# Kernel tuning notes

Hardware: AMD Instinct MI355X
Metric: run time of the kernel (lower is better)

The kernel has to match this reference:

```python
import jax, jax.numpy as jnp
import numpy as np

N = 100000
E = 1600000
NEG_SLOPE = 0.2
EPS = 1e-16


def gat_layer(x, src, dst, w, W, a_src, a_dst, b):
    # x: [N, Cin] -> h: [N, Cout]
    h = x @ W
    alpha_src = h @ a_src  # [N]
    alpha_dst = h @ a_dst  # [N]
    # per-edge score: alpha_j + alpha_i, leaky relu, edge-weight adjustment
    alpha = alpha_src[src] + alpha_dst[dst]
    alpha = jax.nn.leaky_relu(alpha, NEG_SLOPE)
    alpha = alpha + (1.0 - 1.0 / w)
    # segment softmax over destination nodes
    m = jax.ops.segment_max(alpha, dst, num_segments=N)
    ea = jnp.exp(alpha - m[dst])
    denom = jax.ops.segment_sum(ea, dst, num_segments=N)
    alpha = ea / (denom[dst] + EPS)
    # scatter-add aggregation of weighted source features
    out = jax.ops.segment_sum(h[src] * alpha[:, None], dst, num_segments=N)
    return out + b


def setup_inputs() -> dict:
    key = jax.random.key(0)
    ks = jax.random.split(key, 12)
    return {
        "x": jax.random.normal(ks[0], (N, 128), dtype=jnp.float32),
        "edge_index": jax.random.randint(ks[1], (2, E), 0, N, dtype=jnp.int64)
        if jax.config.jax_enable_x64 else jax.random.randint(ks[1], (2, E), 0, N, dtype=jnp.int32),
        "edge_weight": jax.random.uniform(ks[2], (E,), dtype=jnp.float32, minval=0.5, maxval=1.5),
        "W1": jax.random.normal(ks[3], (128, 64), dtype=jnp.float32) * 0.08,
        "a_src1": jax.random.normal(ks[4], (64,), dtype=jnp.float32) * 0.1,
        "a_dst1": jax.random.normal(ks[5], (64,), dtype=jnp.float32) * 0.1,
        "b1": jax.random.normal(ks[6], (64,), dtype=jnp.float32) * 0.01,
        "W2": jax.random.normal(ks[7], (64, 7), dtype=jnp.float32) * 0.12,
        "a_src2": jax.random.normal(ks[8], (7,), dtype=jnp.float32) * 0.1,
        "a_dst2": jax.random.normal(ks[9], (7,), dtype=jnp.float32) * 0.1,
        "b2": jax.random.normal(ks[10], (7,), dtype=jnp.float32) * 0.01,
    }


def reference(x, edge_index, edge_weight, W1, a_src1, a_dst1, b1, W2, a_src2, a_dst2, b2):
    # add self loops with edge weight fill_value=1.0 (GATConv default behavior)
    loop = jnp.arange(N, dtype=edge_index.dtype)
    src = jnp.concatenate([edge_index[0], loop])
    dst = jnp.concatenate([edge_index[1], loop])
    w = jnp.concatenate([edge_weight, jnp.ones((N,), dtype=edge_weight.dtype)])
    h = gat_layer(x, src, dst, w, W1, a_src1, a_dst1, b1)
    h = jax.nn.relu(h)  # dropout is identity in eval mode
    out = gat_layer(h, src, dst, w, W2, a_src2, a_dst2, b2)
    return out
```

## Files before the change

kernel.cpp:

```cpp
#include <hip/hip_runtime.h>
#include <hip/hip_bf16.h>

typedef __hip_bfloat16 bf16;

#define DEPS 1e-16f
#define CAP 32
#define OVF_MAX 131072

__device__ __forceinline__ float bfu_lo(unsigned u) { return __uint_as_float(u << 16); }
__device__ __forceinline__ float bfu_hi(unsigned u) { return __uint_as_float(u & 0xffff0000u); }

__device__ __forceinline__ float dec_wt(unsigned u) {
    return (float)(u & 32767u) * (1.f / 8192.f) - 1.1f;
}

__global__ __launch_bounds__(256) void f_hist(
    const int* __restrict__ dstv, int* __restrict__ cnt,
    unsigned char* __restrict__ rank8, int E)
{
    int e = blockIdx.x * 256 + threadIdx.x;
    if (e >= E) return;
    int d = dstv[e];
    int pos = atomicAdd(&cnt[d], 1);
    rank8[e] = (unsigned char)min(pos, 255);
}

__global__ __launch_bounds__(256) void f_gemm_scat(
    const float* __restrict__ x, const float* __restrict__ W1,
    const float* __restrict__ a_src, const float* __restrict__ a_dst,
    bf16* __restrict__ h1, float* __restrict__ asrc, float* __restrict__ adst,
    const int* __restrict__ srcv, const int* __restrict__ dstv,
    const float* __restrict__ ew, const unsigned char* __restrict__ rank8,
    const int* __restrict__ cnt,
    unsigned* __restrict__ bkt, uint2* __restrict__ ovf, int* __restrict__ ovfn,
    int N, int E, int T, int gG, int gS)
{
    __shared__ __align__(16) float xl[32 * 128];
    int bid = blockIdx.x;
    int r = bid % 13, chunk = bid / 13;
    int tid = threadIdx.x;

    if (r >= 4) {
        int sb = chunk * 9 + (r - 4);
        if (sb >= gS) return;
        int e = sb * 256 + tid;
        if (e >= T) return;
        int s, d, pos; float wt;
        if (e < E) {
            s = srcv[e]; d = dstv[e]; wt = 1.f - 1.f / ew[e];
            pos = rank8[e];
        } else {
            s = d = e - E; wt = 0.f;
            pos = cnt[d];
        }
        unsigned q = (unsigned)((wt + 1.1f) * 8192.f + 0.5f);
        unsigned entry = ((unsigned)s << 15) | q;
        if (pos < CAP) {
            bkt[(size_t)d * CAP + pos] = entry;
        } else {
            int o = atomicAdd(ovfn, 1);
            if (o < OVF_MAX) { uint2 v; v.x = (unsigned)d; v.y = entry; ovf[o] = v; }
        }
        return;
    }
    int gb = chunk * 4 + r;
    if (gb >= gG) return;
    int n0 = gb * 32;
    for (int i = tid; i < 1024; i += 256) {
        int n = n0 + (i >> 5);
        float4 v = {0.f, 0.f, 0.f, 0.f};
        if (n < N) v = ((const float4*)x)[(size_t)n * 32 + (i & 31)];
        ((float4*)xl)[i] = v;
    }
    __syncthreads();
    int w = tid >> 6, c = tid & 63;
    float sa = a_src[c], da = a_dst[c];
    float acc[8] = {0.f, 0.f, 0.f, 0.f, 0.f, 0.f, 0.f, 0.f};
    const float* Wc = W1 + c;
    for (int k4 = 0; k4 < 32; ++k4) {
        float w0 = Wc[(4 * k4 + 0) * 64];
        float w1 = Wc[(4 * k4 + 1) * 64];
        float w2 = Wc[(4 * k4 + 2) * 64];
        float w3 = Wc[(4 * k4 + 3) * 64];
        #pragma unroll
        for (int i = 0; i < 8; ++i) {
            float4 xv = ((const float4*)(xl + (w * 8 + i) * 128))[k4];
            acc[i] = fmaf(xv.x, w0, fmaf(xv.y, w1,
                     fmaf(xv.z, w2, fmaf(xv.w, w3, acc[i]))));
        }
    }
    #pragma unroll
    for (int i = 0; i < 8; ++i) {
        int n = n0 + w * 8 + i;
        float a = acc[i];
        float ps = a * sa, pd = a * da;
        #pragma unroll
        for (int o = 32; o; o >>= 1) {
            ps += __shfl_xor(ps, o);
            pd += __shfl_xor(pd, o);
        }
        if (n < N) {
            h1[(size_t)n * 64 + c] = __float2bfloat16(a);
            if (c == 0) { asrc[n] = ps; adst[n] = pd; }
        }
    }
}

__global__ __launch_bounds__(256) void f_agg1(
    const int* __restrict__ cnt, const unsigned* __restrict__ bkt,
    const uint2* __restrict__ ovf, const int* __restrict__ ovfn,
    const float* __restrict__ asrc, const float* __restrict__ adst,
    const bf16* __restrict__ h1,
    const float* __restrict__ b1, const float* __restrict__ W2,
    const float* __restrict__ a2s, const float* __restrict__ a2d,
    float* __restrict__ h2p, float* __restrict__ ad2, int N)
{
    __shared__ __align__(16) float WxT[16][68];
    __shared__ __align__(16) float b1l[64];
    __shared__ float2 eb[4][64];
    int tid = threadIdx.x;
    if (tid < 64) {
        float us = 0.f, ud = 0.f;
        #pragma unroll
        for (int c = 0; c < 7; ++c) {
            float wv = W2[tid * 7 + c];
            WxT[c][tid] = wv;
            us = fmaf(wv, a2s[c], us);
            ud = fmaf(wv, a2d[c], ud);
        }
        WxT[7][tid] = us;
        WxT[8][tid] = ud;
        #pragma unroll
        for (int r = 9; r < 16; ++r) WxT[r][tid] = 0.f;
        b1l[tid] = b1[tid];
    }
    __syncthreads();
    int d = blockIdx.x * 4 + (tid >> 6);
    int lane = tid & 63;
    if (d >= N) return;
    int lenf = cnt[d] + 1;
    int nc = min(lenf, CAP);
    size_t r0 = (size_t)d * CAP;
    float adv = adst[d];
    int g8 = lane >> 3, l8 = lane & 7;
    float2* ebw = eb[tid >> 6];
    float acc[8] = {0.f, 0.f, 0.f, 0.f, 0.f, 0.f, 0.f, 0.f};
    float sm = 0.f;
    {
        float ea = 0.f; unsigned s = 0;
        if (lane < nc) {
            unsigned u = bkt[r0 + lane];
            s = u >> 15;
            float a = asrc[s] + adv;
            a = (a > 0.f) ? a : 0.2f * a;
            ea = __expf(a + dec_wt(u));
            sm += ea;
        }
        ebw[lane] = make_float2(ea, __uint_as_float(s));
        for (int j = 0; j < nc; j += 8) {
            float2 eq = ebw[j + g8];
            float e = eq.x;
            unsigned sj = __float_as_uint(eq.y);
            uint4 hv = *(const uint4*)&h1[(size_t)sj * 64 + (l8 << 3)];
            acc[0] = fmaf(e, bfu_lo(hv.x), acc[0]);
            acc[1] = fmaf(e, bfu_hi(hv.x), acc[1]);
            acc[2] = fmaf(e, bfu_lo(hv.y), acc[2]);
            acc[3] = fmaf(e, bfu_hi(hv.y), acc[3]);
            acc[4] = fmaf(e, bfu_lo(hv.z), acc[4]);
            acc[5] = fmaf(e, bfu_hi(hv.z), acc[5]);
            acc[6] = fmaf(e, bfu_lo(hv.w), acc[6]);
            acc[7] = fmaf(e, bfu_hi(hv.w), acc[7]);
        }
    }
    if (lenf > CAP) {
        int no = min(*ovfn, OVF_MAX);
        for (int i = g8; i < no; i += 8) {
            uint2 ov = ovf[i];
            if ((int)ov.x == d) {
                unsigned u = ov.y;
                unsigned s = u >> 15;
                float a = asrc[s] + adv;
                a = (a > 0.f) ? a : 0.2f * a;
                float ea = __expf(a + dec_wt(u));
                if (l8 == 0) sm += ea;
                uint4 hv = *(const uint4*)&h1[(size_t)s * 64 + (l8 << 3)];
                acc[0] = fmaf(ea, bfu_lo(hv.x), acc[0]);
                acc[1] = fmaf(ea, bfu_hi(hv.x), acc[1]);
                acc[2] = fmaf(ea, bfu_lo(hv.y), acc[2]);
                acc[3] = fmaf(ea, bfu_hi(hv.y), acc[3]);
                acc[4] = fmaf(ea, bfu_lo(hv.z), acc[4]);
                acc[5] = fmaf(ea, bfu_hi(hv.z), acc[5]);
                acc[6] = fmaf(ea, bfu_lo(hv.w), acc[6]);
                acc[7] = fmaf(ea, bfu_hi(hv.w), acc[7]);
            }
        }
    }
    #pragma unroll
    for (int o = 32; o; o >>= 1) sm += __shfl_xor(sm, o);
    #pragma unroll
    for (int k = 0; k < 8; ++k) {
        acc[k] += __shfl_xor(acc[k], 8);
        acc[k] += __shfl_xor(acc[k], 16);
        acc[k] += __shfl_xor(acc[k], 32);
    }
    float inv = 1.f / (sm + DEPS);
    int c0 = l8 << 3;
    float4 bA = *(const float4*)&b1l[c0];
    float4 bB = *(const float4*)&b1l[c0 + 4];
    float v0 = fmaxf(fmaf(acc[0], inv, bA.x), 0.f);
    float v1 = fmaxf(fmaf(acc[1], inv, bA.y), 0.f);
    float v2 = fmaxf(fmaf(acc[2], inv, bA.z), 0.f);
    float v3 = fmaxf(fmaf(acc[3], inv, bA.w), 0.f);
    float v4 = fmaxf(fmaf(acc[4], inv, bB.x), 0.f);
    float v5 = fmaxf(fmaf(acc[5], inv, bB.y), 0.f);
    float v6 = fmaxf(fmaf(acc[6], inv, bB.z), 0.f);
    float v7 = fmaxf(fmaf(acc[7], inv, bB.w), 0.f);
    float4 wA0 = *(const float4*)&WxT[g8][c0];
    float4 wA1 = *(const float4*)&WxT[g8][c0 + 4];
    float4 wB0 = *(const float4*)&WxT[g8 + 8][c0];
    float4 wB1 = *(const float4*)&WxT[g8 + 8][c0 + 4];
    float rA = fmaf(v0, wA0.x, fmaf(v1, wA0.y, fmaf(v2, wA0.z, fmaf(v3, wA0.w,
               fmaf(v4, wA1.x, fmaf(v5, wA1.y, fmaf(v6, wA1.z, v7 * wA1.w)))))));
    float rB = fmaf(v0, wB0.x, fmaf(v1, wB0.y, fmaf(v2, wB0.z, fmaf(v3, wB0.w,
               fmaf(v4, wB1.x, fmaf(v5, wB1.y, fmaf(v6, wB1.z, v7 * wB1.w)))))));
    rA += __shfl_xor(rA, 1); rA += __shfl_xor(rA, 2); rA += __shfl_xor(rA, 4);
    rB += __shfl_xor(rB, 1); rB += __shfl_xor(rB, 2); rB += __shfl_xor(rB, 4);
    if (l8 == 0) {
        h2p[(size_t)d * 8 + g8] = rA;
        if (g8 == 0) ad2[d] = rB;
    }
}

__global__ __launch_bounds__(256) void f_agg2(
    const int* __restrict__ cnt, const unsigned* __restrict__ bkt,
    const uint2* __restrict__ ovf, const int* __restrict__ ovfn,
    const float* __restrict__ h2p, const float* __restrict__ ad2,
    const float* __restrict__ b2, float* __restrict__ out, int N)
{
    __shared__ float b2l[7];
    if (threadIdx.x < 7) b2l[threadIdx.x] = b2[threadIdx.x];
    __syncthreads();
    int lane = threadIdx.x & 63;
    int wv = threadIdx.x >> 6;
    int grp = lane >> 3, l8 = lane & 7;
    int d = blockIdx.x * 32 + wv * 8 + grp;
    bool valid = d < N;
    int lenf = 0; float adv = 0.f;
    if (valid) { lenf = cnt[d] + 1; adv = ad2[d]; }
    int nc = min(lenf, CAP);
    size_t r0 = (size_t)d * CAP;
    float sm = 0.f;
    float a0 = 0.f, a1 = 0.f, a2 = 0.f, a3 = 0.f, a4 = 0.f, a5 = 0.f, a6 = 0.f;
    for (int p = l8; p < nc; p += 8) {
        unsigned u = bkt[r0 + p];
        int s = (int)(u >> 15);
        const float* hr = &h2p[(size_t)s * 8];
        float4 A = *(const float4*)hr;
        float4 B = *(const float4*)(hr + 4);
        float a = B.w + adv;
        a = (a > 0.f) ? a : 0.2f * a;
        float ea = __expf(a + dec_wt(u));
        sm += ea;
        a0 = fmaf(ea, A.x, a0); a1 = fmaf(ea, A.y, a1);
        a2 = fmaf(ea, A.z, a2); a3 = fmaf(ea, A.w, a3);
        a4 = fmaf(ea, B.x, a4); a5 = fmaf(ea, B.y, a5);
        a6 = fmaf(ea, B.z, a6);
    }
    if (lenf > CAP) {
        int no = min(*ovfn, OVF_MAX);
        for (int i = l8; i < no; i += 8) {
            uint2 ov = ovf[i];
            if ((int)ov.x == d) {
                unsigned u = ov.y;
                int s = (int)(u >> 15);
                const float* hr = &h2p[(size_t)s * 8];
                float4 A = *(const float4*)hr;
                float4 B = *(const float4*)(hr + 4);
                float a = B.w + adv;
                a = (a > 0.f) ? a : 0.2f * a;
                float ea = __expf(a + dec_wt(u));
                sm += ea;
                a0 = fmaf(ea, A.x, a0); a1 = fmaf(ea, A.y, a1);
                a2 = fmaf(ea, A.z, a2); a3 = fmaf(ea, A.w, a3);
                a4 = fmaf(ea, B.x, a4); a5 = fmaf(ea, B.y, a5);
                a6 = fmaf(ea, B.z, a6);
            }
        }
    }
    #pragma unroll
    for (int o = 4; o; o >>= 1) {
        sm += __shfl_xor(sm, o);
        a0 += __shfl_xor(a0, o); a1 += __shfl_xor(a1, o);
        a2 += __shfl_xor(a2, o); a3 += __shfl_xor(a3, o);
        a4 += __shfl_xor(a4, o); a5 += __shfl_xor(a5, o);
        a6 += __shfl_xor(a6, o);
    }
    if (valid && l8 < 7) {
        float inv = 1.f / (sm + DEPS);
        float val = (l8 < 4) ? ((l8 < 2) ? (l8 ? a1 : a0) : ((l8 == 2) ? a2 : a3))
                             : ((l8 < 6) ? ((l8 == 4) ? a4 : a5) : a6);
        out[(size_t)d * 7 + l8] = fmaf(val, inv, b2l[l8]);
    }
}


extern "C" void kernel_launch(void* const* d_in, const int* in_sizes, int n_in,
                              void* d_out, int out_size, void* d_ws, size_t ws_size,
                              hipStream_t stream) {
    const float* x   = (const float*)d_in[0];
    const int*   ei  = (const int*)d_in[1];
    const float* ew  = (const float*)d_in[2];
    const float* W1  = (const float*)d_in[3];
    const float* as1 = (const float*)d_in[4];
    const float* ad1 = (const float*)d_in[5];
    const float* b1  = (const float*)d_in[6];
    const float* W2  = (const float*)d_in[7];
    const float* a2s = (const float*)d_in[8];
    const float* a2d = (const float*)d_in[9];
    const float* b2  = (const float*)d_in[10];

    int N = in_sizes[0] / 128;
    int E = in_sizes[1] / 2;
    int T = E + N;
    const int* srcv = ei;
    const int* dstv = ei + E;
    float* out = (float*)d_out;

    size_t A = 0;
    auto take = [&](size_t b) { size_t o = A; A = (A + b + 255) & ~(size_t)255; return o; };
    size_t o_h1   = take((size_t)N * 64 * 2);
    size_t o_bkt  = take((size_t)N * CAP * 4);
    size_t o_h2p  = take((size_t)N * 8 * 4);
    size_t o_ovf  = take((size_t)OVF_MAX * 8);
    size_t o_cnt  = take((size_t)N * 4);
    size_t o_ovfn = take(256);
    size_t o_asrc = take((size_t)N * 4);
    size_t o_adst = take((size_t)N * 4);
    size_t o_ad2  = take((size_t)N * 4);

    char* base = (char*)d_ws;
    bf16*     h1    = (bf16*)(base + o_h1);
    unsigned* bkt   = (unsigned*)(base + o_bkt);
    float*    h2p   = (float*)(base + o_h2p);
    unsigned char* rank8 = (unsigned char*)(base + o_h2p);
    uint2*    ovf   = (uint2*)(base + o_ovf);
    int*      cnt   = (int*)(base + o_cnt);
    int*      ovfn  = (int*)(base + o_ovfn);
    float*    asrc  = (float*)(base + o_asrc);
    float*    adst  = (float*)(base + o_adst);
    float*    ad2   = (float*)(base + o_ad2);

    int gE = (E + 255) / 256;
    int gG = (N + 31) / 32;
    int gS = (T + 255) / 256;
    int chunks = max((gG + 3) / 4, (gS + 8) / 9);
    int gridGS = chunks * 13;

    hipMemsetAsync(cnt, 0, (size_t)N * 4 + 256, stream);
    f_hist<<<gE, 256, 0, stream>>>(dstv, cnt, rank8, E);
    f_gemm_scat<<<gridGS, 256, 0, stream>>>(x, W1, as1, ad1, h1, asrc, adst,
                                            srcv, dstv, ew, rank8, cnt,
                                            bkt, ovf, ovfn, N, E, T, gG, gS);
    f_agg1 <<<(N + 3) / 4, 256, 0, stream>>>(cnt, bkt, ovf, ovfn, asrc, adst, h1,
                                             b1, W2, a2s, a2d, h2p, ad2, N);
    f_agg2 <<<(N + 31) / 32, 256, 0, stream>>>(cnt, bkt, ovf, ovfn, h2p, ad2, b2, out, N);
}
```

Baseline: 315.0 us.

## Fuse all stages into one cooperative persistent kernel with grid syncs

```diff
diff --git a/kernel.cpp b/kernel.cpp
--- a/kernel.cpp
+++ b/kernel.cpp
@@ -1,6 +1,8 @@
 #include <hip/hip_runtime.h>
 #include <hip/hip_bf16.h>
-
+#include <hip/hip_cooperative_groups.h>
+
+namespace cg = cooperative_groups;
 typedef __hip_bfloat16 bf16;
 
 #define DEPS 1e-16f
@@ -14,264 +16,250 @@
     return (float)(u & 32767u) * (1.f / 8192.f) - 1.1f;
 }
 
-__global__ __launch_bounds__(256) void f_hist(
-    const int* __restrict__ dstv, int* __restrict__ cnt,
-    unsigned char* __restrict__ rank8, int E)
+__global__ __launch_bounds__(256) void f_mega(
+    const float* __restrict__ x, const int* __restrict__ srcv,
+    const int* __restrict__ dstv, const float* __restrict__ ew,
+    const float* __restrict__ W1, const float* __restrict__ as1,
+    const float* __restrict__ ad1, const float* __restrict__ b1,
+    const float* __restrict__ W2, const float* __restrict__ a2s,
+    const float* __restrict__ a2d, const float* __restrict__ b2,
+    bf16* __restrict__ h1, unsigned* __restrict__ bkt,
+    float* __restrict__ h2p, unsigned char* __restrict__ rank8,
+    uint2* __restrict__ ovf, int* __restrict__ cnt, int* __restrict__ ovfn,
+    float* __restrict__ asrc, float* __restrict__ adst, float* __restrict__ ad2,
+    float* __restrict__ out, int N, int E, int T)
 {
-    int e = blockIdx.x * 256 + threadIdx.x;
-    if (e >= E) return;
-    int d = dstv[e];
-    int pos = atomicAdd(&cnt[d], 1);
-    rank8[e] = (unsigned char)min(pos, 255);
-}
-
-__global__ __launch_bounds__(256) void f_gemm_scat(
-    const float* __restrict__ x, const float* __restrict__ W1,
-    const float* __restrict__ a_src, const float* __restrict__ a_dst,
-    bf16* __restrict__ h1, float* __restrict__ asrc, float* __restrict__ adst,
-    const int* __restrict__ srcv, const int* __restrict__ dstv,
-    const float* __restrict__ ew, const unsigned char* __restrict__ rank8,
-    const int* __restrict__ cnt,
-    unsigned* __restrict__ bkt, uint2* __restrict__ ovf, int* __restrict__ ovfn,
-    int N, int E, int T, int gG, int gS)
-{
-    __shared__ __align__(16) float xl[32 * 128];
-    int bid = blockIdx.x;
-    int r = bid % 13, chunk = bid / 13;
+    cg::grid_group grid = cg::this_grid();
+    __shared__ __align__(16) char smem[16896];
     int tid = threadIdx.x;
-
-    if (r >= 4) {
-        int sb = chunk * 9 + (r - 4);
-        if (sb >= gS) return;
-        int e = sb * 256 + tid;
-        if (e >= T) return;
-        int s, d, pos; float wt;
-        if (e < E) {
-            s = srcv[e]; d = dstv[e]; wt = 1.f - 1.f / ew[e];
-            pos = rank8[e];
-        } else {
-            s = d = e - E; wt = 0.f;
-            pos = cnt[d];
-        }
+    int gid = blockIdx.x * 256 + tid;
+    int nth = gridDim.x * 256;
+
+    for (int i = gid; i < N; i += nth) cnt[i] = 0;
+    if (gid == 0) *ovfn = 0;
+    grid.sync();
+
+    {
+        float* xl = (float*)smem;
+        int gG = (N + 31) >> 5;
+        int gH = (T + 255) >> 8;
+        int chunks = max((gG + 3) / 4, (gH + 8) / 9);
+        int V = chunks * 13;
+        for (int vb = blockIdx.x; vb < V; vb += gridDim.x) {
+            int r = vb % 13, chunk = vb / 13;
+            if (r >= 4) {
+                int hb = chunk * 9 + (r - 4);
+                if (hb >= gH) continue;
+                int e = hb * 256 + tid;
+                if (e >= T) continue;
+                if (e < E) {
+                    int d = dstv[e];
+                    int pos = atomicAdd(&cnt[d], 1);
+                    rank8[e] = (unsigned char)min(pos, 255);
+                } else {
+                    int d = e - E;
+                    unsigned q = (unsigned)((0.f + 1.1f) * 8192.f + 0.5f);
+                    bkt[(size_t)d * CAP] = ((unsigned)d << 15) | q;
+                }
+            } else {
+                int gb = chunk * 4 + r;
+                if (gb >= gG) continue;
+                int n0 = gb * 32;
+                for (int i = tid; i < 1024; i += 256) {
+                    int n = n0 + (i >> 5);
+                    float4 v = {0.f, 0.f, 0.f, 0.f};
+                    if (n < N) v = ((const float4*)x)[(size_t)n * 32 + (i & 31)];
+                    ((float4*)xl)[i] = v;
+                }
+                __syncthreads();
+                int wv = tid >> 6, c = tid & 63;
+                float sa = as1[c], da = ad1[c];
+                float acc[8] = {0.f, 0.f, 0.f, 0.f, 0.f, 0.f, 0.f, 0.f};
+                const float* Wc = W1 + c;
+                for (int k4 = 0; k4 < 32; ++k4) {
+                    float w0 = Wc[(4 * k4 + 0) * 64];
+                    float w1 = Wc[(4 * k4 + 1) * 64];
+                    float w2 = Wc[(4 * k4 + 2) * 64];
+                    float w3 = Wc[(4 * k4 + 3) * 64];
+                    #pragma unroll
+                    for (int i = 0; i < 8; ++i) {
+                        float4 xv = ((const float4*)(xl + (wv * 8 + i) * 128))[k4];
+                        acc[i] = fmaf(xv.x, w0, fmaf(xv.y, w1,
+                                 fmaf(xv.z, w2, fmaf(xv.w, w3, acc[i]))));
+                    }
+                }
+                #pragma unroll
+                for (int i = 0; i < 8; ++i) {
+                    int n = n0 + wv * 8 + i;
+                    float a = acc[i];
+                    float ps = a * sa, pd = a * da;
+                    #pragma unroll
+                    for (int o = 32; o; o >>= 1) {
+                        ps += __shfl_xor(ps, o);
+                        pd += __shfl_xor(pd, o);
+                    }
+                    if (n < N) {
+                        h1[(size_t)n * 64 + c] = __float2bfloat16(a);
+                        if (c == 0) { asrc[n] = ps; adst[n] = pd; }
+                    }
+                }
+                __syncthreads();
+            }
+        }
+    }
+    grid.sync();
+
+    for (int e = gid; e < E; e += nth) {
+        int s = srcv[e], d = dstv[e];
+        float wt = 1.f - 1.f / ew[e];
         unsigned q = (unsigned)((wt + 1.1f) * 8192.f + 0.5f);
         unsigned entry = ((unsigned)s << 15) | q;
+        int pos = 1 + (int)rank8[e];
         if (pos < CAP) {
             bkt[(size_t)d * CAP + pos] = entry;
         } else {
             int o = atomicAdd(ovfn, 1);
             if (o < OVF_MAX) { uint2 v; v.x = (unsigned)d; v.y = entry; ovf[o] = v; }
         }
-        return;
-    }
-    int gb = chunk * 4 + r;
-    if (gb >= gG) return;
-    int n0 = gb * 32;
-    for (int i = tid; i < 1024; i += 256) {
-        int n = n0 + (i >> 5);
-        float4 v = {0.f, 0.f, 0.f, 0.f};
-        if (n < N) v = ((const float4*)x)[(size_t)n * 32 + (i & 31)];
-        ((float4*)xl)[i] = v;
-    }
-    __syncthreads();
-    int w = tid >> 6, c = tid & 63;
-    float sa = a_src[c], da = a_dst[c];
-    float acc[8] = {0.f, 0.f, 0.f, 0.f, 0.f, 0.f, 0.f, 0.f};
-    const float* Wc = W1 + c;
-    for (int k4 = 0; k4 < 32; ++k4) {
-        float w0 = Wc[(4 * k4 + 0) * 64];
-        float w1 = Wc[(4 * k4 + 1) * 64];
-        float w2 = Wc[(4 * k4 + 2) * 64];
-        float w3 = Wc[(4 * k4 + 3) * 64];
-        #pragma unroll
-        for (int i = 0; i < 8; ++i) {
-            float4 xv = ((const float4*)(xl + (w * 8 + i) * 128))[k4];
-            acc[i] = fmaf(xv.x, w0, fmaf(xv.y, w1,
-                     fmaf(xv.z, w2, fmaf(xv.w, w3, acc[i]))));
-        }
-    }
-    #pragma unroll
-    for (int i = 0; i < 8; ++i) {
-        int n = n0 + w * 8 + i;
-        float a = acc[i];
-        float ps = a * sa, pd = a * da;
-        #pragma unroll
-        for (int o = 32; o; o >>= 1) {
-            ps += __shfl_xor(ps, o);
-            pd += __shfl_xor(pd, o);
-        }
-        if (n < N) {
-            h1[(size_t)n * 64 + c] = __float2bfloat16(a);
-            if (c == 0) { asrc[n] = ps; adst[n] = pd; }
-        }
-    }
-}
-
-__global__ __launch_bounds__(256) void f_agg1(
-    const int* __restrict__ cnt, const unsigned* __restrict__ bkt,
-    const uint2* __restrict__ ovf, const int* __restrict__ ovfn,
-    const float* __restrict__ asrc, const float* __restrict__ adst,
-    const bf16* __restrict__ h1,
-    const float* __restrict__ b1, const float* __restrict__ W2,
-    const float* __restrict__ a2s, const float* __restrict__ a2d,
-    float* __restrict__ h2p, float* __restrict__ ad2, int N)
-{
-    __shared__ __align__(16) float WxT[16][68];
-    __shared__ __align__(16) float b1l[64];
-    __shared__ float2 eb[4][64];
-    int tid = threadIdx.x;
-    if (tid < 64) {
-        float us = 0.f, ud = 0.f;
-        #pragma unroll
-        for (int c = 0; c < 7; ++c) {
-            float wv = W2[tid * 7 + c];
-            WxT[c][tid] = wv;
-            us = fmaf(wv, a2s[c], us);
-            ud = fmaf(wv, a2d[c], ud);
-        }
-        WxT[7][tid] = us;
-        WxT[8][tid] = ud;
-        #pragma unroll
-        for (int r = 9; r < 16; ++r) WxT[r][tid] = 0.f;
-        b1l[tid] = b1[tid];
-    }
-    __syncthreads();
-    int d = blockIdx.x * 4 + (tid >> 6);
-    int lane = tid & 63;
-    if (d >= N) return;
-    int lenf = cnt[d] + 1;
-    int nc = min(lenf, CAP);
-    size_t r0 = (size_t)d * CAP;
-    float adv = adst[d];
-    int g8 = lane >> 3, l8 = lane & 7;
-    float2* ebw = eb[tid >> 6];
-    float acc[8] = {0.f, 0.f, 0.f, 0.f, 0.f, 0.f, 0.f, 0.f};
-    float sm = 0.f;
+    }
+    grid.sync();
+
     {
-        float ea = 0.f; unsigned s = 0;
-        if (lane < nc) {
-            unsigned u = bkt[r0 + lane];
-            s = u >> 15;
-            float a = asrc[s] + adv;
-            a = (a > 0.f) ? a : 0.2f * a;
-            ea = __expf(a + dec_wt(u));
-            sm += ea;
-        }
-        ebw[lane] = make_float2(ea, __uint_as_float(s));
-        for (int j = 0; j < nc; j += 8) {
-            float2 eq = ebw[j + g8];
-            float e = eq.x;
-            unsigned sj = __float_as_uint(eq.y);
-            uint4 hv = *(const uint4*)&h1[(size_t)sj * 64 + (l8 << 3)];
-            acc[0] = fmaf(e, bfu_lo(hv.x), acc[0]);
-            acc[1] = fmaf(e, bfu_hi(hv.x), acc[1]);
-            acc[2] = fmaf(e, bfu_lo(hv.y), acc[2]);
-            acc[3] = fmaf(e, bfu_hi(hv.y), acc[3]);
-            acc[4] = fmaf(e, bfu_lo(hv.z), acc[4]);
-            acc[5] = fmaf(e, bfu_hi(hv.z), acc[5]);
-            acc[6] = fmaf(e, bfu_lo(hv.w), acc[6]);
-            acc[7] = fmaf(e, bfu_hi(hv.w), acc[7]);
-        }
-    }
-    if (lenf > CAP) {
-        int no = min(*ovfn, OVF_MAX);
-        for (int i = g8; i < no; i += 8) {
-            uint2 ov = ovf[i];
-            if ((int)ov.x == d) {
-                unsigned u = ov.y;
-                unsigned s = u >> 15;
-                float a = asrc[s] + adv;
-                a = (a > 0.f) ? a : 0.2f * a;
-                float ea = __expf(a + dec_wt(u));
-                if (l8 == 0) sm += ea;
-                uint4 hv = *(const uint4*)&h1[(size_t)s * 64 + (l8 << 3)];
-                acc[0] = fmaf(ea, bfu_lo(hv.x), acc[0]);
-                acc[1] = fmaf(ea, bfu_hi(hv.x), acc[1]);
-                acc[2] = fmaf(ea, bfu_lo(hv.y), acc[2]);
-                acc[3] = fmaf(ea, bfu_hi(hv.y), acc[3]);
-                acc[4] = fmaf(ea, bfu_lo(hv.z), acc[4]);
-                acc[5] = fmaf(ea, bfu_hi(hv.z), acc[5]);
-                acc[6] = fmaf(ea, bfu_lo(hv.w), acc[6]);
-                acc[7] = fmaf(ea, bfu_hi(hv.w), acc[7]);
-            }
-        }
-    }
-    #pragma unroll
-    for (int o = 32; o; o >>= 1) sm += __shfl_xor(sm, o);
-    #pragma unroll
-    for (int k = 0; k < 8; ++k) {
-        acc[k] += __shfl_xor(acc[k], 8);
-        acc[k] += __shfl_xor(acc[k], 16);
-        acc[k] += __shfl_xor(acc[k], 32);
-    }
-    float inv = 1.f / (sm + DEPS);
-    int c0 = l8 << 3;
-    float4 bA = *(const float4*)&b1l[c0];
-    float4 bB = *(const float4*)&b1l[c0 + 4];
-    float v0 = fmaxf(fmaf(acc[0], inv, bA.x), 0.f);
-    float v1 = fmaxf(fmaf(acc[1], inv, bA.y), 0.f);
-    float v2 = fmaxf(fmaf(acc[2], inv, bA.z), 0.f);
-    float v3 = fmaxf(fmaf(acc[3], inv, bA.w), 0.f);
-    float v4 = fmaxf(fmaf(acc[4], inv, bB.x), 0.f);
-    float v5 = fmaxf(fmaf(acc[5], inv, bB.y), 0.f);
-    float v6 = fmaxf(fmaf(acc[6], inv, bB.z), 0.f);
-    float v7 = fmaxf(fmaf(acc[7], inv, bB.w), 0.f);
-    float4 wA0 = *(const float4*)&WxT[g8][c0];
-    float4 wA1 = *(const float4*)&WxT[g8][c0 + 4];
-    float4 wB0 = *(const float4*)&WxT[g8 + 8][c0];
-    float4 wB1 = *(const float4*)&WxT[g8 + 8][c0 + 4];
-    float rA = fmaf(v0, wA0.x, fmaf(v1, wA0.y, fmaf(v2, wA0.z, fmaf(v3, wA0.w,
-               fmaf(v4, wA1.x, fmaf(v5, wA1.y, fmaf(v6, wA1.z, v7 * wA1.w)))))));
-    float rB = fmaf(v0, wB0.x, fmaf(v1, wB0.y, fmaf(v2, wB0.z, fmaf(v3, wB0.w,
-               fmaf(v4, wB1.x, fmaf(v5, wB1.y, fmaf(v6, wB1.z, v7 * wB1.w)))))));
-    rA += __shfl_xor(rA, 1); rA += __shfl_xor(rA, 2); rA += __shfl_xor(rA, 4);
-    rB += __shfl_xor(rB, 1); rB += __shfl_xor(rB, 2); rB += __shfl_xor(rB, 4);
-    if (l8 == 0) {
-        h2p[(size_t)d * 8 + g8] = rA;
-        if (g8 == 0) ad2[d] = rB;
-    }
-}
-
-__global__ __launch_bounds__(256) void f_agg2(
-    const int* __restrict__ cnt, const unsigned* __restrict__ bkt,
-    const uint2* __restrict__ ovf, const int* __restrict__ ovfn,
-    const float* __restrict__ h2p, const float* __restrict__ ad2,
-    const float* __restrict__ b2, float* __restrict__ out, int N)
-{
-    __shared__ float b2l[7];
-    if (threadIdx.x < 7) b2l[threadIdx.x] = b2[threadIdx.x];
-    __syncthreads();
-    int lane = threadIdx.x & 63;
-    int wv = threadIdx.x >> 6;
-    int grp = lane >> 3, l8 = lane & 7;
-    int d = blockIdx.x * 32 + wv * 8 + grp;
-    bool valid = d < N;
-    int lenf = 0; float adv = 0.f;
-    if (valid) { lenf = cnt[d] + 1; adv = ad2[d]; }
-    int nc = min(lenf, CAP);
-    size_t r0 = (size_t)d * CAP;
-    float sm = 0.f;
-    float a0 = 0.f, a1 = 0.f, a2 = 0.f, a3 = 0.f, a4 = 0.f, a5 = 0.f, a6 = 0.f;
-    for (int p = l8; p < nc; p += 8) {
-        unsigned u = bkt[r0 + p];
-        int s = (int)(u >> 15);
-        const float* hr = &h2p[(size_t)s * 8];
-        float4 A = *(const float4*)hr;
-        float4 B = *(const float4*)(hr + 4);
-        float a = B.w + adv;
-        a = (a > 0.f) ? a : 0.2f * a;
-        float ea = __expf(a + dec_wt(u));
-        sm += ea;
-        a0 = fmaf(ea, A.x, a0); a1 = fmaf(ea, A.y, a1);
-        a2 = fmaf(ea, A.z, a2); a3 = fmaf(ea, A.w, a3);
-        a4 = fmaf(ea, B.x, a4); a5 = fmaf(ea, B.y, a5);
-        a6 = fmaf(ea, B.z, a6);
-    }
-    if (lenf > CAP) {
-        int no = min(*ovfn, OVF_MAX);
-        for (int i = l8; i < no; i += 8) {
-            uint2 ov = ovf[i];
-            if ((int)ov.x == d) {
-                unsigned u = ov.y;
+        float (*WxT)[68] = (float(*)[68])smem;
+        float* b1l = (float*)(smem + 4352);
+        float2 (*eb)[64] = (float2(*)[64])(smem + 4608);
+        if (tid < 64) {
+            float us = 0.f, ud = 0.f;
+            #pragma unroll
+            for (int c = 0; c < 7; ++c) {
+                float wv = W2[tid * 7 + c];
+                WxT[c][tid] = wv;
+                us = fmaf(wv, a2s[c], us);
+                ud = fmaf(wv, a2d[c], ud);
+            }
+            WxT[7][tid] = us;
+            WxT[8][tid] = ud;
+            #pragma unroll
+            for (int r = 9; r < 16; ++r) WxT[r][tid] = 0.f;
+            b1l[tid] = b1[tid];
+        }
+        __syncthreads();
+        int lane = tid & 63, wid = tid >> 6;
+        int g8 = lane >> 3, l8 = lane & 7;
+        float2* ebw = eb[wid];
+        for (int dbase = blockIdx.x * 4; dbase < N; dbase += gridDim.x * 4) {
+            int d = dbase + wid;
+            if (d >= N) continue;
+            int lenf = cnt[d] + 1;
+            int nc = min(lenf, CAP);
+            size_t r0 = (size_t)d * CAP;
+            float adv = adst[d];
+            float acc[8] = {0.f, 0.f, 0.f, 0.f, 0.f, 0.f, 0.f, 0.f};
+            float sm = 0.f;
+            {
+                float ea = 0.f; unsigned s = 0;
+                if (lane < nc) {
+                    unsigned u = bkt[r0 + lane];
+                    s = u >> 15;
+                    float a = asrc[s] + adv;
+                    a = (a > 0.f) ? a : 0.2f * a;
+                    ea = __expf(a + dec_wt(u));
+                    sm += ea;
+                }
+                ebw[lane] = make_float2(ea, __uint_as_float(s));
+                for (int j = 0; j < nc; j += 8) {
+                    float2 eq = ebw[j + g8];
+                    float e = eq.x;
+                    unsigned sj = __float_as_uint(eq.y);
+                    uint4 hv = *(const uint4*)&h1[(size_t)sj * 64 + (l8 << 3)];
+                    acc[0] = fmaf(e, bfu_lo(hv.x), acc[0]);
+                    acc[1] = fmaf(e, bfu_hi(hv.x), acc[1]);
+                    acc[2] = fmaf(e, bfu_lo(hv.y), acc[2]);
+                    acc[3] = fmaf(e, bfu_hi(hv.y), acc[3]);
+                    acc[4] = fmaf(e, bfu_lo(hv.z), acc[4]);
+                    acc[5] = fmaf(e, bfu_hi(hv.z), acc[5]);
+                    acc[6] = fmaf(e, bfu_lo(hv.w), acc[6]);
+                    acc[7] = fmaf(e, bfu_hi(hv.w), acc[7]);
+                }
+            }
+            if (lenf > CAP) {
+                int no = min(*ovfn, OVF_MAX);
+                for (int i = g8; i < no; i += 8) {
+                    uint2 ov = ovf[i];
+                    if ((int)ov.x == d) {
+                        unsigned u = ov.y;
+                        unsigned s = u >> 15;
+                        float a = asrc[s] + adv;
+                        a = (a > 0.f) ? a : 0.2f * a;
+                        float ea = __expf(a + dec_wt(u));
+                        if (l8 == 0) sm += ea;
+                        uint4 hv = *(const uint4*)&h1[(size_t)s * 64 + (l8 << 3)];
+                        acc[0] = fmaf(ea, bfu_lo(hv.x), acc[0]);
+                        acc[1] = fmaf(ea, bfu_hi(hv.x), acc[1]);
+                        acc[2] = fmaf(ea, bfu_lo(hv.y), acc[2]);
+                        acc[3] = fmaf(ea, bfu_hi(hv.y), acc[3]);
+                        acc[4] = fmaf(ea, bfu_lo(hv.z), acc[4]);
+                        acc[5] = fmaf(ea, bfu_hi(hv.z), acc[5]);
+                        acc[6] = fmaf(ea, bfu_lo(hv.w), acc[6]);
+                        acc[7] = fmaf(ea, bfu_hi(hv.w), acc[7]);
+                    }
+                }
+            }
+            #pragma unroll
+            for (int o = 32; o; o >>= 1) sm += __shfl_xor(sm, o);
+            #pragma unroll
+            for (int k = 0; k < 8; ++k) {
+                acc[k] += __shfl_xor(acc[k], 8);
+                acc[k] += __shfl_xor(acc[k], 16);
+                acc[k] += __shfl_xor(acc[k], 32);
+            }
+            float inv = 1.f / (sm + DEPS);
+            int c0 = l8 << 3;
+            float4 bA = *(const float4*)&b1l[c0];
+            float4 bB = *(const float4*)&b1l[c0 + 4];
+            float v0 = fmaxf(fmaf(acc[0], inv, bA.x), 0.f);
+            float v1 = fmaxf(fmaf(acc[1], inv, bA.y), 0.f);
+            float v2 = fmaxf(fmaf(acc[2], inv, bA.z), 0.f);
+            float v3 = fmaxf(fmaf(acc[3], inv, bA.w), 0.f);
+            float v4 = fmaxf(fmaf(acc[4], inv, bB.x), 0.f);
+            float v5 = fmaxf(fmaf(acc[5], inv, bB.y), 0.f);
+            float v6 = fmaxf(fmaf(acc[6], inv, bB.z), 0.f);
+            float v7 = fmaxf(fmaf(acc[7], inv, bB.w), 0.f);
+            float4 wA0 = *(const float4*)&WxT[g8][c0];
+            float4 wA1 = *(const float4*)&WxT[g8][c0 + 4];
+            float4 wB0 = *(const float4*)&WxT[g8 + 8][c0];
+            float4 wB1 = *(const float4*)&WxT[g8 + 8][c0 + 4];
+            float rA = fmaf(v0, wA0.x, fmaf(v1, wA0.y, fmaf(v2, wA0.z, fmaf(v3, wA0.w,
+                       fmaf(v4, wA1.x, fmaf(v5, wA1.y, fmaf(v6, wA1.z, v7 * wA1.w)))))));
+            float rB = fmaf(v0, wB0.x, fmaf(v1, wB0.y, fmaf(v2, wB0.z, fmaf(v3, wB0.w,
+                       fmaf(v4, wB1.x, fmaf(v5, wB1.y, fmaf(v6, wB1.z, v7 * wB1.w)))))));
+            rA += __shfl_xor(rA, 1); rA += __shfl_xor(rA, 2); rA += __shfl_xor(rA, 4);
+            rB += __shfl_xor(rB, 1); rB += __shfl_xor(rB, 2); rB += __shfl_xor(rB, 4);
+            if (l8 == 0) {
+                h2p[(size_t)d * 8 + g8] = rA;
+                if (g8 == 0) ad2[d] = rB;
+            }
+        }
+    }
+    grid.sync();
+
+    {
+        float* b2l = (float*)smem;
+        if (tid < 7) b2l[tid] = b2[tid];
+        __syncthreads();
+        int lane = tid & 63, wv = tid >> 6;
+        int grp = lane >> 3, l8 = lane & 7;
+        for (int dbase = blockIdx.x * 32; dbase < N; dbase += gridDim.x * 32) {
+            int d = dbase + wv * 8 + grp;
+            bool valid = d < N;
+            int lenf = 0; float adv = 0.f;
+            if (valid) { lenf = cnt[d] + 1; adv = ad2[d]; }
+            int nc = min(lenf, CAP);
+            size_t r0 = (size_t)d * CAP;
+            float sm = 0.f;
+            float a0 = 0.f, a1 = 0.f, a2 = 0.f, a3 = 0.f, a4 = 0.f, a5 = 0.f, a6 = 0.f;
+            for (int p = l8; p < nc; p += 8) {
+                unsigned u = bkt[r0 + p];
                 int s = (int)(u >> 15);
                 const float* hr = &h2p[(size_t)s * 8];
                 float4 A = *(const float4*)hr;
@@ -285,21 +273,42 @@
                 a4 = fmaf(ea, B.x, a4); a5 = fmaf(ea, B.y, a5);
                 a6 = fmaf(ea, B.z, a6);
             }
-        }
-    }
-    #pragma unroll
-    for (int o = 4; o; o >>= 1) {
-        sm += __shfl_xor(sm, o);
-        a0 += __shfl_xor(a0, o); a1 += __shfl_xor(a1, o);
-        a2 += __shfl_xor(a2, o); a3 += __shfl_xor(a3, o);
-        a4 += __shfl_xor(a4, o); a5 += __shfl_xor(a5, o);
-        a6 += __shfl_xor(a6, o);
-    }
-    if (valid && l8 < 7) {
-        float inv = 1.f / (sm + DEPS);
-        float val = (l8 < 4) ? ((l8 < 2) ? (l8 ? a1 : a0) : ((l8 == 2) ? a2 : a3))
-                             : ((l8 < 6) ? ((l8 == 4) ? a4 : a5) : a6);
-        out[(size_t)d * 7 + l8] = fmaf(val, inv, b2l[l8]);
+            if (lenf > CAP) {
+                int no = min(*ovfn, OVF_MAX);
+                for (int i = l8; i < no; i += 8) {
+                    uint2 ov = ovf[i];
+                    if ((int)ov.x == d) {
+                        unsigned u = ov.y;
+                        int s = (int)(u >> 15);
+                        const float* hr = &h2p[(size_t)s * 8];
+                        float4 A = *(const float4*)hr;
+                        float4 B = *(const float4*)(hr + 4);
+                        float a = B.w + adv;
+                        a = (a > 0.f) ? a : 0.2f * a;
+                        float ea = __expf(a + dec_wt(u));
+                        sm += ea;
+                        a0 = fmaf(ea, A.x, a0); a1 = fmaf(ea, A.y, a1);
+                        a2 = fmaf(ea, A.z, a2); a3 = fmaf(ea, A.w, a3);
+                        a4 = fmaf(ea, B.x, a4); a5 = fmaf(ea, B.y, a5);
+                        a6 = fmaf(ea, B.z, a6);
+                    }
+                }
+            }
+            #pragma unroll
+            for (int o = 4; o; o >>= 1) {
+                sm += __shfl_xor(sm, o);
+                a0 += __shfl_xor(a0, o); a1 += __shfl_xor(a1, o);
+                a2 += __shfl_xor(a2, o); a3 += __shfl_xor(a3, o);
+                a4 += __shfl_xor(a4, o); a5 += __shfl_xor(a5, o);
+                a6 += __shfl_xor(a6, o);
+            }
+            if (valid && l8 < 7) {
+                float inv = 1.f / (sm + DEPS);
+                float val = (l8 < 4) ? ((l8 < 2) ? (l8 ? a1 : a0) : ((l8 == 2) ? a2 : a3))
+                                     : ((l8 < 6) ? ((l8 == 4) ? a4 : a5) : a6);
+                out[(size_t)d * 7 + l8] = fmaf(val, inv, b2l[l8]);
+            }
+        }
     }
 }
 
@@ -350,18 +359,29 @@
     float*    adst  = (float*)(base + o_adst);
     float*    ad2   = (float*)(base + o_ad2);
 
-    int gE = (E + 255) / 256;
-    int gG = (N + 31) / 32;
-    int gS = (T + 255) / 256;
-    int chunks = max((gG + 3) / 4, (gS + 8) / 9);
-    int gridGS = chunks * 13;
-
-    hipMemsetAsync(cnt, 0, (size_t)N * 4 + 256, stream);
-    f_hist<<<gE, 256, 0, stream>>>(dstv, cnt, rank8, E);
-    f_gemm_scat<<<gridGS, 256, 0, stream>>>(x, W1, as1, ad1, h1, asrc, adst,
-                                            srcv, dstv, ew, rank8, cnt,
-                                            bkt, ovf, ovfn, N, E, T, gG, gS);
-    f_agg1 <<<(N + 3) / 4, 256, 0, stream>>>(cnt, bkt, ovf, ovfn, asrc, adst, h1,
-                                             b1, W2, a2s, a2d, h2p, ad2, N);
-    f_agg2 <<<(N + 31) / 32, 256, 0, stream>>>(cnt, bkt, ovf, ovfn, h2p, ad2, b2, out, N);
+    static int maxBlocks = 0;
+    if (maxBlocks == 0) {
+        int perCU = 0;
+        if (hipOccupancyMaxActiveBlocksPerMultiprocessor(&perCU, f_mega, 256, 0)
+                != hipSuccess || perCU <= 0)
+            perCU = 2;
+        int dev = 0, nCU = 0;
+        hipGetDevice(&dev);
+        if (hipDeviceGetAttribute(&nCU, hipDeviceAttributeMultiprocessorCount, dev)
+                != hipSuccess || nCU <= 0)
+            nCU = 256;
+        maxBlocks = perCU * nCU;
+    }
+
+    void* args[] = {
+        (void*)&x, (void*)&srcv, (void*)&dstv, (void*)&ew,
+        (void*)&W1, (void*)&as1, (void*)&ad1, (void*)&b1,
+        (void*)&W2, (void*)&a2s, (void*)&a2d, (void*)&b2,
+        (void*)&h1, (void*)&bkt, (void*)&h2p, (void*)&rank8,
+        (void*)&ovf, (void*)&cnt, (void*)&ovfn,
+        (void*)&asrc, (void*)&adst, (void*)&ad2,
+        (void*)&out, (void*)&N, (void*)&E, (void*)&T
+    };
+    hipLaunchCooperativeKernel((const void*)f_mega, dim3(maxBlocks), dim3(256),
+                               args, 0, stream);
 }
```

After: 633.6 us. +101.1%, slower.
